# Optimization experiments

Hardware: AMD Instinct MI355X
Metric: run time of the kernel (lower is better)

Reference implementation:

```python
import jax, jax.numpy as jnp
import numpy as np

N_HEADS = 16


def setup_inputs() -> dict:
    key = jax.random.key(0)
    ks = jax.random.split(key, 7)
    B, S, D = 2, 2048, 1024
    x = jax.random.normal(ks[0], (B, S, D), dtype=jnp.float32)
    attn_mask = jax.random.normal(ks[1], (S, S), dtype=jnp.float32) * 0.1
    attn_bias = jax.random.normal(ks[2], (B, S, S), dtype=jnp.float32) * 0.1
    Wqkv = jax.random.normal(ks[3], (D, 3 * D), dtype=jnp.float32) * (D ** -0.5)
    bqkv = jnp.zeros((3 * D,), dtype=jnp.float32)
    Wout = jax.random.normal(ks[4], (D, D), dtype=jnp.float32) * (D ** -0.5)
    bout = jnp.zeros((D,), dtype=jnp.float32)
    return {"x": x, "attn_mask": attn_mask, "attn_bias": attn_bias,
            "Wqkv": Wqkv, "bqkv": bqkv, "Wout": Wout, "bout": bout}


def reference(x, attn_mask, attn_bias, Wqkv, bqkv, Wout, bout):
    B, S, D = x.shape
    H = N_HEADS
    hd = D // H
    # qkv projection: [B,S,3D] -> [3,B,H,S,hd]
    qkv = (x @ Wqkv + bqkv).reshape(B, S, 3, H, hd).transpose(2, 0, 3, 1, 4)
    q, k, v = qkv[0], qkv[1], qkv[2]
    scores = jnp.einsum('bhqd,bhkd->bhqk', q, k) / (hd ** 0.5)
    scores = scores + attn_mask[None, None, :, :] + attn_bias[:, None, :, :]
    attn = jax.nn.softmax(scores, axis=-1)  # dropout p=0.0 (eval)
    out = jnp.einsum('bhqk,bhkd->bhqd', attn, v)
    out = out.transpose(0, 2, 1, 3).reshape(B, S, D)
    return out @ Wout + bout
```

## Files before the change

kernel.cpp:

```cpp
#include <hip/hip_runtime.h>
#include <hip/hip_bf16.h>


#define S_LEN 2048
#define DMODEL 1024
#define NH 16
#define HD 64

typedef __bf16 bf16x8 __attribute__((ext_vector_type(8)));
typedef __bf16 bf16x4 __attribute__((ext_vector_type(4)));
typedef __bf16 bf16x2v __attribute__((ext_vector_type(2)));
typedef float f32x4 __attribute__((ext_vector_type(4)));
typedef short s16x4 __attribute__((ext_vector_type(4)));

#define GLD_LDS16(g, l)                                              \
  __builtin_amdgcn_global_load_lds(                                  \
      (const __attribute__((address_space(1))) unsigned int*)(g),    \
      (__attribute__((address_space(3))) unsigned int*)(l), 16, 0, 0)

#if __has_builtin(__builtin_amdgcn_mfma_f32_16x16x16bf16_1k)
#define HAVE_MFMA_16x16x16_BF16 1
#else
#define HAVE_MFMA_16x16x16_BF16 0
#endif

#if __has_builtin(__builtin_amdgcn_exp2f)
#define EXP2F(x) __builtin_amdgcn_exp2f(x)
#else
static __device__ __forceinline__ float EXP2F(float x) {
  float r;
  asm volatile("v_exp_f32 %0, %1" : "=v"(r) : "v"(x));
  return r;
}
#endif

#define LOG2E 1.44269504f

__global__ __launch_bounds__(256) void preprocess(
    const float* __restrict__ x, const float* __restrict__ mask,
    const float* __restrict__ bias, const float* __restrict__ Wqkv,
    const float* __restrict__ Wout, __bf16* __restrict__ Xb,
    __bf16* __restrict__ Wt, __bf16* __restrict__ Wt2,
    __bf16* __restrict__ MB) {
  __shared__ __align__(16) char smem[64 * 65 * 4];
  const int bid = blockIdx.x;
  const int tid = threadIdx.x;

  if (bid < 4096) {
    int i = bid * 256 + tid;
    float4 v = ((const float4*)x)[i];
    bf16x4 o = {(__bf16)v.x, (__bf16)v.y, (__bf16)v.z, (__bf16)v.w};
    *(bf16x4*)&Xb[(size_t)i * 4] = o;
  } else if (bid < 5120) {
    const float* W;
    __bf16* Wo;
    int ncols, n0, k0;
    if (bid < 4864) {
      int id = bid - 4096;
      W = Wqkv; Wo = Wt; ncols = 3072;
      n0 = (id % 48) * 64; k0 = (id / 48) * 64;
    } else {
      int id = bid - 4864;
      W = Wout; Wo = Wt2; ncols = 1024;
      n0 = (id & 15) * 64; k0 = (id >> 4) * 64;
    }
    float(*tile)[65] = (float(*)[65])smem;
    {
      int c = tid & 63, r4 = tid >> 6;
#pragma unroll
      for (int p = 0; p < 16; ++p) {
        int r = r4 + p * 4;
        tile[r][c] = W[(size_t)(k0 + r) * ncols + n0 + c];
      }
    }
    __syncthreads();
    {
      int cc = (tid & 31) * 2, r8 = tid >> 5;
#pragma unroll
      for (int p = 0; p < 8; ++p) {
        int rr = r8 + p * 8;
        bf16x2v o = {(__bf16)tile[cc][rr], (__bf16)tile[cc + 1][rr]};
        *(bf16x2v*)&Wo[(size_t)(n0 + rr) * 1024 + k0 + cc] = o;
      }
    }
  } else {
    int id = bid - 5120;
    const int kt = id & 31, qt = id >> 5;
    __bf16(*sm)[68] = (__bf16(*)[68])smem;
    const int r0 = tid >> 4;
    const int cc = (tid & 15) * 4;
    const float* mrow = mask + (size_t)(qt * 64) * S_LEN + kt * 64;
    float4 mld[4];
#pragma unroll
    for (int p = 0; p < 4; ++p)
      mld[p] = *(const float4*)(mrow + (size_t)(r0 + p * 16) * S_LEN + cc);
    const int w = tid >> 6, lane = tid & 63;
    const int quad = lane >> 4, cl = lane & 15;
    for (int b = 0; b < 2; ++b) {
      const float* brow =
          bias + ((size_t)b * S_LEN + qt * 64) * S_LEN + kt * 64;
#pragma unroll
      for (int p = 0; p < 4; ++p) {
        int r = r0 + p * 16;
        float4 a = *(const float4*)(brow + (size_t)r * S_LEN + cc);
        sm[r][cc + 0] = (__bf16)((mld[p].x + a.x) * LOG2E);
        sm[r][cc + 1] = (__bf16)((mld[p].y + a.y) * LOG2E);
        sm[r][cc + 2] = (__bf16)((mld[p].z + a.z) * LOG2E);
        sm[r][cc + 3] = (__bf16)((mld[p].w + a.w) * LOG2E);
      }
      __syncthreads();
      __bf16 vals[16];
#pragma unroll
      for (int ct = 0; ct < 4; ++ct) {
        bf16x4 v = *(const bf16x4*)&sm[w * 16 + cl][ct * 16 + quad * 4];
        *(bf16x4*)&vals[ct * 4] = v;
      }
      __bf16* op = MB + (((size_t)(b * 32 + qt) * 32 + kt) * 4096) +
                   (w * 64 + lane) * 16;
      *(bf16x8*)op = *(bf16x8*)&vals[0];
      *(bf16x8*)(op + 8) = *(bf16x8*)&vals[8];
      __syncthreads();
    }
  }
}

__global__ __launch_bounds__(256) void gemm_qkv_mfma(
    const __bf16* __restrict__ Xb, const __bf16* __restrict__ Wt,
    const float* __restrict__ bqkv, __bf16* __restrict__ Qb,
    __bf16* __restrict__ Kb, __bf16* __restrict__ Vtb) {
  __shared__ __align__(16) __bf16 shm[4 * 64 * 72];
  __bf16* As = shm;
  __bf16* Bs = shm + 4096;
  const int tid = threadIdx.x;
  const int w = tid >> 6, lane = tid & 63;
  const int c = lane & 15, quad = lane >> 4;
  const int wm = w >> 1, wn = w & 1;
  const int rowBase = blockIdx.y * 128;
  const int colBase = blockIdx.x * 128;

  f32x4 acc[4][4] = {};

  const __bf16* gA0 =
      Xb + (size_t)(rowBase + w * 32 + (lane >> 2)) * 1024 + (lane & 3) * 8;
  const __bf16* gB0 =
      Wt + (size_t)(colBase + w * 32 + (lane >> 2)) * 1024 + (lane & 3) * 8;
  __bf16* lA0 = &As[(w * 32) * 32];
  __bf16* lB0 = &Bs[(w * 32) * 32];

  for (int k0 = 0; k0 < 1024; k0 += 32) {
    __syncthreads();
#pragma unroll
    for (int p = 0; p < 2; ++p) {
      GLD_LDS16(gA0 + (size_t)p * 16 * 1024 + k0, lA0 + p * 16 * 32);
      GLD_LDS16(gB0 + (size_t)p * 16 * 1024 + k0, lB0 + p * 16 * 32);
    }
    __syncthreads();

    bf16x8 af[4], bfr[4];
#pragma unroll
    for (int mt = 0; mt < 4; ++mt)
      af[mt] = *(const bf16x8*)&As[(wm * 64 + mt * 16 + c) * 32 + quad * 8];
#pragma unroll
    for (int nt = 0; nt < 4; ++nt)
      bfr[nt] = *(const bf16x8*)&Bs[(wn * 64 + nt * 16 + c) * 32 + quad * 8];
#pragma unroll
    for (int mt = 0; mt < 4; ++mt)
#pragma unroll
      for (int nt = 0; nt < 4; ++nt)
        acc[mt][nt] = __builtin_amdgcn_mfma_f32_16x16x32_bf16(
            af[mt], bfr[nt], acc[mt][nt], 0, 0, 0);
  }

  if (colBase < 2048) {
#pragma unroll
    for (int mt = 0; mt < 4; ++mt) {
      int row0 = rowBase + wm * 64 + mt * 16 + quad * 4;
#pragma unroll
      for (int nt = 0; nt < 4; ++nt) {
        int col = colBase + wn * 64 + nt * 16 + c;
        float bias = bqkv[col];
        int three = col >> 10;
        int h = (col & 1023) >> 6;
        int d = col & 63;
#pragma unroll
        for (int r = 0; r < 4; ++r) {
          int rr = row0 + r;
          int bb = rr >> 11, s = rr & 2047;
          float val = acc[mt][nt][r] + bias;
          size_t ho = (size_t)(bb * NH + h);
          if (three == 0)
            Qb[(ho * S_LEN + s) * HD + d] = (__bf16)val;
          else
            Kb[(ho * S_LEN + s) * HD + d] = (__bf16)val;
        }
      }
    }
  } else {
    __syncthreads();
    __bf16* Tt = shm + w * (64 * 72);
    const int cols0 = colBase + wn * 64;
    const int rows0 = rowBase + wm * 64;
    const int hq = (cols0 & 1023) >> 6;
    const int bb = rows0 >> 11;
    const int sBase = rows0 & 2047;
#pragma unroll
    for (int nt = 0; nt < 4; ++nt) {
      float bias = bqkv[cols0 + nt * 16 + c];
#pragma unroll
      for (int mt = 0; mt < 4; ++mt) {
        __bf16 t4[4];
#pragma unroll
        for (int r = 0; r < 4; ++r) t4[r] = (__bf16)(acc[mt][nt][r] + bias);
        *(bf16x4*)&Tt[(nt * 16 + c) * 72 + mt * 16 + quad * 4] =
            *(bf16x4*)t4;
      }
    }
    __syncthreads();
    const size_t vbase = ((size_t)(bb * NH + hq) * HD) * S_LEN;
    const int s0 = (lane & 7) * 8;
    const int dl0 = lane >> 3;
#pragma unroll
    for (int dt = 0; dt < 8; ++dt) {
      int dl = dt * 8 + dl0;
      bf16x8 v = *(const bf16x8*)&Tt[dl * 72 + s0];
      *(bf16x8*)&Vtb[vbase + (size_t)dl * S_LEN + sBase + s0] = v;
    }
  }
}

__global__ __launch_bounds__(256, 3) void attn_mfma(
    const __bf16* __restrict__ Qb, const __bf16* __restrict__ Kb,
    const __bf16* __restrict__ Vtb, const __bf16* __restrict__ MB,
    __bf16* __restrict__ PO, float* __restrict__ L) {
  const int qt = blockIdx.x, h = blockIdx.y;
  const int b = blockIdx.z >> 1, half = blockIdx.z & 1;
  const int tid = threadIdx.x;
  const int w = tid >> 6;
  const int lane = tid & 63;
  const int c = lane & 15;
  const int quad = lane >> 4;

  __shared__ __align__(16) __bf16 Ks[2][64 * 64];
  __shared__ __align__(16) __bf16 Vs[2][64 * 64];
#if !HAVE_MFMA_16x16x16_BF16
  __shared__ __align__(16) __bf16 P2[4][16 * 72];
#endif

  const size_t headoff = (size_t)(b * NH + h) * S_LEN * HD;
  const int kv0 = half * 1024;
  const __bf16* Qg = Qb + headoff + (size_t)(qt * 128) * HD;
  const __bf16* Kg = Kb + headoff + (size_t)kv0 * HD;
  const __bf16* Vg = Vtb + headoff;
  const __bf16* mbp0 = MB +
                       ((size_t)(b * 32 + qt * 2 + 0) * 32 + half * 16) * 4096 +
                       (w * 64 + lane) * 16;
  const __bf16* mbp1 = MB +
                       ((size_t)(b * 32 + qt * 2 + 1) * 32 + half * 16) * 4096 +
                       (w * 64 + lane) * 16;

  __bf16* POx = PO + (size_t)half * 4194304;
  float* Lx = L + half * 65536;

  const int f0 = tid >> 3, f1 = f0 + 32;
  const int j = tid & 7;
  const int sj0 = j ^ (f0 & 7);
  const int sj1 = j ^ (f1 & 7);
  const int lds0 = tid * 8;
  const int lds1 = (256 + tid) * 8;

  bf16x8 qa[2][2];
#pragma unroll
  for (int g = 0; g < 2; ++g) {
    qa[g][0] = *(const bf16x8*)(Qg + (g * 64 + w * 16 + c) * HD + quad * 8);
    qa[g][1] =
        *(const bf16x8*)(Qg + (g * 64 + w * 16 + c) * HD + quad * 8 + 32);
  }

  const int rs0 = (quad ^ (c & 7)) * 8;
  const int rs1 = ((quad + 4) ^ (c & 7)) * 8;

  f32x4 Oa[2][4] = {};
  f32x4 psum[2] = {};

  GLD_LDS16(Kg + (size_t)f0 * HD + sj0 * 8, &Ks[0][lds0]);
  GLD_LDS16(Kg + (size_t)f1 * HD + sj1 * 8, &Ks[0][lds1]);
  GLD_LDS16(Vg + (size_t)f0 * S_LEN + kv0 + sj0 * 8, &Vs[0][lds0]);
  GLD_LDS16(Vg + (size_t)f1 * S_LEN + kv0 + sj1 * 8, &Vs[0][lds1]);

  const __bf16* kgp0 = Kg + (size_t)(64 + f0) * HD + sj0 * 8;
  const __bf16* kgp1 = Kg + (size_t)(64 + f1) * HD + sj1 * 8;
  const __bf16* vgp0 = Vg + (size_t)f0 * S_LEN + kv0 + 64 + sj0 * 8;
  const __bf16* vgp1 = Vg + (size_t)f1 * S_LEN + kv0 + 64 + sj1 * 8;

  bf16x8 rMB[2][2];
  rMB[0][0] = *(const bf16x8*)mbp0;
  rMB[0][1] = *(const bf16x8*)(mbp0 + 8);
  rMB[1][0] = *(const bf16x8*)mbp1;
  rMB[1][1] = *(const bf16x8*)(mbp1 + 8);
  mbp0 += 4096;
  mbp1 += 4096;

  __syncthreads();

  const float c1 = 0.125f * LOG2E;

#pragma unroll 2
  for (int t = 0; t < 16; ++t) {
    const int cur = t & 1, nxt = cur ^ 1;
    if (t < 15) {
      GLD_LDS16(kgp0, &Ks[nxt][lds0]);
      GLD_LDS16(kgp1, &Ks[nxt][lds1]);
      GLD_LDS16(vgp0, &Vs[nxt][lds0]);
      GLD_LDS16(vgp1, &Vs[nxt][lds1]);
    }
    kgp0 += 64 * HD;
    kgp1 += 64 * HD;
    vgp0 += 64;
    vgp1 += 64;

    bf16x8 kf0[4], kf1[4];
#pragma unroll
    for (int ct = 0; ct < 4; ++ct) {
      kf0[ct] = *(const bf16x8*)&Ks[cur][(ct * 16 + c) * 64 + rs0];
      kf1[ct] = *(const bf16x8*)&Ks[cur][(ct * 16 + c) * 64 + rs1];
    }

    s16x4 pb[2][4];
#pragma unroll
    for (int g = 0; g < 2; ++g) {
      f32x4 sv[4];
      __builtin_amdgcn_s_setprio(1);
#pragma unroll
      for (int ct = 0; ct < 4; ++ct) {
        f32x4 a = {};
        a = __builtin_amdgcn_mfma_f32_16x16x32_bf16(kf0[ct], qa[g][0], a, 0,
                                                    0, 0);
        a = __builtin_amdgcn_mfma_f32_16x16x32_bf16(kf1[ct], qa[g][1], a, 0,
                                                    0, 0);
        sv[ct] = a;
      }
      __builtin_amdgcn_s_setprio(0);
#pragma unroll
      for (int ct = 0; ct < 4; ++ct) {
        f32x4 pv;
#pragma unroll
        for (int r = 0; r < 4; ++r) {
          float mb = (ct < 2) ? (float)rMB[g][0][ct * 4 + r]
                              : (float)rMB[g][1][(ct - 2) * 4 + r];
          pv[r] = EXP2F(sv[ct][r] * c1 + mb);
        }
        psum[g] += pv;
        __bf16 t4[4];
#pragma unroll
        for (int r = 0; r < 4; ++r) t4[r] = (__bf16)pv[r];
        pb[g][ct] = *(s16x4*)t4;
      }
      const __bf16* mp = g ? mbp1 : mbp0;
      rMB[g][0] = *(const bf16x8*)mp;
      rMB[g][1] = *(const bf16x8*)(mp + 8);
    }
    mbp0 += 4096;
    mbp1 += 4096;

#if HAVE_MFMA_16x16x16_BF16
    s16x4 vf[4][4];
#pragma unroll
    for (int ft = 0; ft < 4; ++ft) {
      const int fr = ft * 16 + c;
#pragma unroll
      for (int ct = 0; ct < 4; ++ct) {
        const int chunk = ((ct * 2 + (quad >> 1)) ^ (fr & 7)) * 8 +
                          (quad & 1) * 4;
        vf[ft][ct] = *(const s16x4*)&Vs[cur][fr * 64 + chunk];
      }
    }
    __builtin_amdgcn_s_setprio(1);
#pragma unroll
    for (int g = 0; g < 2; ++g)
#pragma unroll
      for (int ft = 0; ft < 4; ++ft)
#pragma unroll
        for (int ct = 0; ct < 4; ++ct)
          Oa[g][ft] = __builtin_amdgcn_mfma_f32_16x16x16bf16_1k(
              vf[ft][ct], pb[g][ct], Oa[g][ft], 0, 0, 0);
    __builtin_amdgcn_s_setprio(0);
#else
#pragma unroll
    for (int g = 0; g < 2; ++g) {
#pragma unroll
      for (int ct = 0; ct < 4; ++ct)
        *(bf16x4*)&P2[w][c * 72 + ct * 16 + quad * 4] = *(bf16x4*)&pb[g][ct];
      bf16x8 pf0 = *(const bf16x8*)&P2[w][c * 72 + quad * 8];
      bf16x8 pf1 = *(const bf16x8*)&P2[w][c * 72 + 32 + quad * 8];
#pragma unroll
      for (int ft = 0; ft < 4; ++ft) {
        const int fr = ft * 16 + c;
        bf16x8 vv0 = *(const bf16x8*)&Vs[cur][fr * 64 + rs0];
        bf16x8 vv1 = *(const bf16x8*)&Vs[cur][fr * 64 + rs1];
        Oa[g][ft] = __builtin_amdgcn_mfma_f32_16x16x32_bf16(vv0, pf0,
                                                            Oa[g][ft], 0, 0, 0);
        Oa[g][ft] = __builtin_amdgcn_mfma_f32_16x16x32_bf16(vv1, pf1,
                                                            Oa[g][ft], 0, 0, 0);
      }
    }
#endif

    __syncthreads();
  }

#pragma unroll
  for (int g = 0; g < 2; ++g) {
    float lsum = psum[g][0] + psum[g][1] + psum[g][2] + psum[g][3];
    lsum += __shfl_xor(lsum, 16);
    lsum += __shfl_xor(lsum, 32);
    if (lane < 16)
      Lx[(size_t)(b * NH + h) * S_LEN + qt * 128 + g * 64 + w * 16 + c] = lsum;
    __bf16* orow = POx +
                   (size_t)(b * S_LEN + qt * 128 + g * 64 + w * 16 + c) *
                       DMODEL +
                   h * HD;
#pragma unroll
    for (int ft = 0; ft < 4; ++ft) {
      __bf16 t4[4];
#pragma unroll
      for (int r = 0; r < 4; ++r) t4[r] = (__bf16)Oa[g][ft][r];
      *(bf16x4*)(orow + ft * 16 + quad * 4) = *(bf16x4*)t4;
    }
  }
}

__global__ __launch_bounds__(256) void combine(const __bf16* __restrict__ PO,
                                               const float* __restrict__ L,
                                               __bf16* __restrict__ AOb) {
  const int i = blockIdx.x * 256 + threadIdx.x;
  const size_t e = (size_t)i * 8;
  const int hidx = (int)(e >> 6) & 15;
  const int s = (int)(e >> 10) & 2047;
  const int b = (int)(e >> 21);
  const size_t li = ((size_t)(b * NH + hidx) << 11) + s;
  const float invl = 1.0f / (L[li] + L[65536 + li]);
  bf16x8 a = *(const bf16x8*)&PO[e];
  bf16x8 c = *(const bf16x8*)&PO[4194304 + e];
  __bf16 o[8];
#pragma unroll
  for (int k = 0; k < 8; ++k)
    o[k] = (__bf16)(((float)a[k] + (float)c[k]) * invl);
  *(bf16x8*)&AOb[e] = *(bf16x8*)o;
}

__global__ __launch_bounds__(256) void gemm_out_mfma(
    const __bf16* __restrict__ AOb, const __bf16* __restrict__ Wt2,
    const float* __restrict__ bout, float* __restrict__ Out) {
  __shared__ __align__(16) __bf16 As[128 * 32];
  __shared__ __align__(16) __bf16 Bs[64 * 32];
  const int tid = threadIdx.x;
  const int w = tid >> 6, lane = tid & 63;
  const int c = lane & 15, quad = lane >> 4;
  const int rowBase = blockIdx.y * 128;
  const int colBase = blockIdx.x * 64;

  f32x4 acc[2][4] = {};

  const __bf16* gA0 =
      AOb + (size_t)(rowBase + w * 32 + (lane >> 2)) * 1024 + (lane & 3) * 8;
  const __bf16* gB0 =
      Wt2 + (size_t)(colBase + w * 16 + (lane >> 2)) * 1024 + (lane & 3) * 8;
  __bf16* lA0 = &As[(w * 32) * 32];
  __bf16* lB0 = &Bs[(w * 16) * 32];

  for (int k0 = 0; k0 < 1024; k0 += 32) {
    __syncthreads();
#pragma unroll
    for (int p = 0; p < 2; ++p)
      GLD_LDS16(gA0 + (size_t)p * 16 * 1024 + k0, lA0 + p * 16 * 32);
    GLD_LDS16(gB0 + k0, lB0);
    __syncthreads();

    bf16x8 af[2], bfr[4];
#pragma unroll
    for (int mt = 0; mt < 2; ++mt)
      af[mt] = *(const bf16x8*)&As[(w * 32 + mt * 16 + c) * 32 + quad * 8];
#pragma unroll
    for (int nt = 0; nt < 4; ++nt)
      bfr[nt] = *(const bf16x8*)&Bs[(nt * 16 + c) * 32 + quad * 8];
#pragma unroll
    for (int mt = 0; mt < 2; ++mt)
#pragma unroll
      for (int nt = 0; nt < 4; ++nt)
        acc[mt][nt] = __builtin_amdgcn_mfma_f32_16x16x32_bf16(
            af[mt], bfr[nt], acc[mt][nt], 0, 0, 0);
  }

#pragma unroll
  for (int mt = 0; mt < 2; ++mt) {
    int row0 = rowBase + w * 32 + mt * 16 + quad * 4;
#pragma unroll
    for (int nt = 0; nt < 4; ++nt) {
      int col = colBase + nt * 16 + c;
      float bias = bout[col];
#pragma unroll
      for (int r = 0; r < 4; ++r)
        Out[(size_t)(row0 + r) * 1024 + col] = acc[mt][nt][r] + bias;
    }
  }
}

extern "C" void kernel_launch(void* const* d_in, const int* in_sizes, int n_in,
                              void* d_out, int out_size, void* d_ws,
                              size_t ws_size, hipStream_t stream) {
  const float* x = (const float*)d_in[0];
  const float* attn_mask = (const float*)d_in[1];
  const float* attn_bias = (const float*)d_in[2];
  const float* Wqkv = (const float*)d_in[3];
  const float* bqkv = (const float*)d_in[4];
  const float* Wout = (const float*)d_in[5];
  const float* bout = (const float*)d_in[6];
  float* out = (float*)d_out;

  __bf16* base = (__bf16*)d_ws;
  __bf16* Xb = base;
  __bf16* PO = base;
  __bf16* Wt = base + 4194304;
  __bf16* Qb = base + 8388608;
  __bf16* Kb = base + 12582912;
  __bf16* Vtb = base + 16777216;
  __bf16* AOb = base + 16777216;
  __bf16* MB = base + 20971520;
  __bf16* Wt2 = base + 29360128;
  float* Lf = (float*)d_out;

  preprocess<<<6144, 256, 0, stream>>>(x, attn_mask, attn_bias, Wqkv, Wout,
                                       Xb, Wt, Wt2, MB);
  gemm_qkv_mfma<<<dim3(24, 32), 256, 0, stream>>>(Xb, Wt, bqkv, Qb, Kb, Vtb);
  attn_mfma<<<dim3(16, NH, 4), 256, 0, stream>>>(Qb, Kb, Vtb, MB, PO, Lf);
  combine<<<2048, 256, 0, stream>>>(PO, Lf, AOb);
  gemm_out_mfma<<<dim3(16, 32), 256, 0, stream>>>(AOb, Wt2, bout, out);
}
```

Before: 263.2 us.

## Drop split-KV attention and combine kernel; iterate full KV with staggered start

The attention kernel now walks all 32 KV tiles per block, where before it split the KV range into two halves. It normalizes the output in-kernel and writes AOb directly, so the separate combine kernel and the partial-output and L buffers go away. Blocks start at tile 0 or 16 depending on (qt+h) parity to spread memory traffic, and the per-iteration __syncthreads is replaced by a partial vmcnt wait plus a raw s_barrier. The trade is half as many blocks (512) with twice the loop length, which reduces parallelism for latency hiding. The launch_bounds occupancy hint of 3 is also removed.

```diff
diff --git a/kernel.cpp b/kernel.cpp
--- a/kernel.cpp
+++ b/kernel.cpp
@@ -228,12 +228,11 @@
   }
 }
 
-__global__ __launch_bounds__(256, 3) void attn_mfma(
+__global__ __launch_bounds__(256) void attn_mfma(
     const __bf16* __restrict__ Qb, const __bf16* __restrict__ Kb,
     const __bf16* __restrict__ Vtb, const __bf16* __restrict__ MB,
-    __bf16* __restrict__ PO, float* __restrict__ L) {
-  const int qt = blockIdx.x, h = blockIdx.y;
-  const int b = blockIdx.z >> 1, half = blockIdx.z & 1;
+    __bf16* __restrict__ AOb) {
+  const int qt = blockIdx.x, h = blockIdx.y, b = blockIdx.z;
   const int tid = threadIdx.x;
   const int w = tid >> 6;
   const int lane = tid & 63;
@@ -247,19 +246,15 @@
 #endif
 
   const size_t headoff = (size_t)(b * NH + h) * S_LEN * HD;
-  const int kv0 = half * 1024;
   const __bf16* Qg = Qb + headoff + (size_t)(qt * 128) * HD;
-  const __bf16* Kg = Kb + headoff + (size_t)kv0 * HD;
+  const __bf16* Kg = Kb + headoff;
   const __bf16* Vg = Vtb + headoff;
-  const __bf16* mbp0 = MB +
-                       ((size_t)(b * 32 + qt * 2 + 0) * 32 + half * 16) * 4096 +
-                       (w * 64 + lane) * 16;
-  const __bf16* mbp1 = MB +
-                       ((size_t)(b * 32 + qt * 2 + 1) * 32 + half * 16) * 4096 +
-                       (w * 64 + lane) * 16;
-
-  __bf16* POx = PO + (size_t)half * 4194304;
-  float* Lx = L + half * 65536;
+  const __bf16* MBq0 =
+      MB + ((size_t)(b * 32 + qt * 2 + 0) * 32) * 4096 + (w * 64 + lane) * 16;
+  const __bf16* MBq1 =
+      MB + ((size_t)(b * 32 + qt * 2 + 1) * 32) * 4096 + (w * 64 + lane) * 16;
+
+  const int start = ((qt + h) & 1) << 4;
 
   const int f0 = tid >> 3, f1 = f0 + 32;
   const int j = tid & 7;
@@ -267,6 +262,10 @@
   const int sj1 = j ^ (f1 & 7);
   const int lds0 = tid * 8;
   const int lds1 = (256 + tid) * 8;
+  const int kA0 = f0 * HD + sj0 * 8;
+  const int kA1 = f1 * HD + sj1 * 8;
+  const int vA0 = f0 * S_LEN + sj0 * 8;
+  const int vA1 = f1 * S_LEN + sj1 * 8;
 
   bf16x8 qa[2][2];
 #pragma unroll
@@ -282,41 +281,31 @@
   f32x4 Oa[2][4] = {};
   f32x4 psum[2] = {};
 
-  GLD_LDS16(Kg + (size_t)f0 * HD + sj0 * 8, &Ks[0][lds0]);
-  GLD_LDS16(Kg + (size_t)f1 * HD + sj1 * 8, &Ks[0][lds1]);
-  GLD_LDS16(Vg + (size_t)f0 * S_LEN + kv0 + sj0 * 8, &Vs[0][lds0]);
-  GLD_LDS16(Vg + (size_t)f1 * S_LEN + kv0 + sj1 * 8, &Vs[0][lds1]);
-
-  const __bf16* kgp0 = Kg + (size_t)(64 + f0) * HD + sj0 * 8;
-  const __bf16* kgp1 = Kg + (size_t)(64 + f1) * HD + sj1 * 8;
-  const __bf16* vgp0 = Vg + (size_t)f0 * S_LEN + kv0 + 64 + sj0 * 8;
-  const __bf16* vgp1 = Vg + (size_t)f1 * S_LEN + kv0 + 64 + sj1 * 8;
+  GLD_LDS16(Kg + (size_t)start * 64 * HD + kA0, &Ks[0][lds0]);
+  GLD_LDS16(Kg + (size_t)start * 64 * HD + kA1, &Ks[0][lds1]);
+  GLD_LDS16(Vg + (size_t)start * 64 + vA0, &Vs[0][lds0]);
+  GLD_LDS16(Vg + (size_t)start * 64 + vA1, &Vs[0][lds1]);
 
   bf16x8 rMB[2][2];
-  rMB[0][0] = *(const bf16x8*)mbp0;
-  rMB[0][1] = *(const bf16x8*)(mbp0 + 8);
-  rMB[1][0] = *(const bf16x8*)mbp1;
-  rMB[1][1] = *(const bf16x8*)(mbp1 + 8);
-  mbp0 += 4096;
-  mbp1 += 4096;
+  rMB[0][0] = *(const bf16x8*)(MBq0 + (size_t)start * 4096);
+  rMB[0][1] = *(const bf16x8*)(MBq0 + (size_t)start * 4096 + 8);
+  rMB[1][0] = *(const bf16x8*)(MBq1 + (size_t)start * 4096);
+  rMB[1][1] = *(const bf16x8*)(MBq1 + (size_t)start * 4096 + 8);
 
   __syncthreads();
 
   const float c1 = 0.125f * LOG2E;
 
 #pragma unroll 2
-  for (int t = 0; t < 16; ++t) {
+  for (int t = 0; t < 32; ++t) {
     const int cur = t & 1, nxt = cur ^ 1;
-    if (t < 15) {
-      GLD_LDS16(kgp0, &Ks[nxt][lds0]);
-      GLD_LDS16(kgp1, &Ks[nxt][lds1]);
-      GLD_LDS16(vgp0, &Vs[nxt][lds0]);
-      GLD_LDS16(vgp1, &Vs[nxt][lds1]);
-    }
-    kgp0 += 64 * HD;
-    kgp1 += 64 * HD;
-    vgp0 += 64;
-    vgp1 += 64;
+    const int ktn = (start + t + 1) & 31;
+    if (t < 31) {
+      GLD_LDS16(Kg + (size_t)ktn * 64 * HD + kA0, &Ks[nxt][lds0]);
+      GLD_LDS16(Kg + (size_t)ktn * 64 * HD + kA1, &Ks[nxt][lds1]);
+      GLD_LDS16(Vg + (size_t)ktn * 64 + vA0, &Vs[nxt][lds0]);
+      GLD_LDS16(Vg + (size_t)ktn * 64 + vA1, &Vs[nxt][lds1]);
+    }
 
     bf16x8 kf0[4], kf1[4];
 #pragma unroll
@@ -355,12 +344,11 @@
         for (int r = 0; r < 4; ++r) t4[r] = (__bf16)pv[r];
         pb[g][ct] = *(s16x4*)t4;
       }
-      const __bf16* mp = g ? mbp1 : mbp0;
+      const __bf16* mp =
+          (g ? MBq1 : MBq0) + (size_t)ktn * 4096;
       rMB[g][0] = *(const bf16x8*)mp;
       rMB[g][1] = *(const bf16x8*)(mp + 8);
     }
-    mbp0 += 4096;
-    mbp1 += 4096;
 
 #if HAVE_MFMA_16x16x16_BF16
     s16x4 vf[4][4];
@@ -405,7 +393,10 @@
     }
 #endif
 
-    __syncthreads();
+    asm volatile("s_waitcnt vmcnt(4)" ::: "memory");
+    __builtin_amdgcn_sched_barrier(0);
+    __builtin_amdgcn_s_barrier();
+    __builtin_amdgcn_sched_barrier(0);
   }
 
 #pragma unroll
@@ -413,9 +404,8 @@
     float lsum = psum[g][0] + psum[g][1] + psum[g][2] + psum[g][3];
     lsum += __shfl_xor(lsum, 16);
     lsum += __shfl_xor(lsum, 32);
-    if (lane < 16)
-      Lx[(size_t)(b * NH + h) * S_LEN + qt * 128 + g * 64 + w * 16 + c] = lsum;
-    __bf16* orow = POx +
+    const float invl = 1.0f / lsum;
+    __bf16* orow = AOb +
                    (size_t)(b * S_LEN + qt * 128 + g * 64 + w * 16 + c) *
                        DMODEL +
                    h * HD;
@@ -423,29 +413,10 @@
     for (int ft = 0; ft < 4; ++ft) {
       __bf16 t4[4];
 #pragma unroll
-      for (int r = 0; r < 4; ++r) t4[r] = (__bf16)Oa[g][ft][r];
+      for (int r = 0; r < 4; ++r) t4[r] = (__bf16)(Oa[g][ft][r] * invl);
       *(bf16x4*)(orow + ft * 16 + quad * 4) = *(bf16x4*)t4;
     }
   }
-}
-
-__global__ __launch_bounds__(256) void combine(const __bf16* __restrict__ PO,
-                                               const float* __restrict__ L,
-                                               __bf16* __restrict__ AOb) {
-  const int i = blockIdx.x * 256 + threadIdx.x;
-  const size_t e = (size_t)i * 8;
-  const int hidx = (int)(e >> 6) & 15;
-  const int s = (int)(e >> 10) & 2047;
-  const int b = (int)(e >> 21);
-  const size_t li = ((size_t)(b * NH + hidx) << 11) + s;
-  const float invl = 1.0f / (L[li] + L[65536 + li]);
-  bf16x8 a = *(const bf16x8*)&PO[e];
-  bf16x8 c = *(const bf16x8*)&PO[4194304 + e];
-  __bf16 o[8];
-#pragma unroll
-  for (int k = 0; k < 8; ++k)
-    o[k] = (__bf16)(((float)a[k] + (float)c[k]) * invl);
-  *(bf16x8*)&AOb[e] = *(bf16x8*)o;
 }
 
 __global__ __launch_bounds__(256) void gemm_out_mfma(
@@ -519,20 +490,17 @@
 
   __bf16* base = (__bf16*)d_ws;
   __bf16* Xb = base;
-  __bf16* PO = base;
+  __bf16* AOb = base;
   __bf16* Wt = base + 4194304;
   __bf16* Qb = base + 8388608;
   __bf16* Kb = base + 12582912;
   __bf16* Vtb = base + 16777216;
-  __bf16* AOb = base + 16777216;
   __bf16* MB = base + 20971520;
   __bf16* Wt2 = base + 29360128;
-  float* Lf = (float*)d_out;
 
   preprocess<<<6144, 256, 0, stream>>>(x, attn_mask, attn_bias, Wqkv, Wout,
                                        Xb, Wt, Wt2, MB);
   gemm_qkv_mfma<<<dim3(24, 32), 256, 0, stream>>>(Xb, Wt, bqkv, Qb, Kb, Vtb);
-  attn_mfma<<<dim3(16, NH, 4), 256, 0, stream>>>(Qb, Kb, Vtb, MB, PO, Lf);
-  combine<<<2048, 256, 0, stream>>>(PO, Lf, AOb);
+  attn_mfma<<<dim3(16, NH, 2), 256, 0, stream>>>(Qb, Kb, Vtb, MB, AOb);
   gemm_out_mfma<<<dim3(16, 32), 256, 0, stream>>>(AOb, Wt2, bout, out);
 }
```

Measured after the change: 259.1 us. Within noise of the previous version (-1.6%).
